# Kernel tuning notes

Hardware: AMD Instinct MI355X
Metric: run time of the kernel (lower is better)

The kernel has to match this reference:

```python
import jax, jax.numpy as jnp
import numpy as np

B, C, D, H = 2, 1024, 1024, 16
DH = D // H
EPS = 1e-8


def setup_inputs() -> dict:
    key = jax.random.key(0)
    ks = jax.random.split(key, 12)
    s = 0.02
    return {
        "x": jax.random.normal(ks[0], (B, C, D), dtype=jnp.float32),
        "rms_w": jnp.ones((C, D), dtype=jnp.float32),
        "rms_b": jnp.zeros((C, D), dtype=jnp.float32),
        "Wqkv": jax.random.normal(ks[1], (3 * D, D), dtype=jnp.float32) * s,
        "Wout": jax.random.normal(ks[2], (D, D), dtype=jnp.float32) * s,
        "bout": jnp.zeros((D,), dtype=jnp.float32),
        "Wf": jax.random.normal(ks[3], (D, D), dtype=jnp.float32) * s,
        "bf": jnp.zeros((D,), dtype=jnp.float32),
        "Ww": jax.random.normal(ks[4], (D, D), dtype=jnp.float32) * s,
        "bw": jnp.zeros((D,), dtype=jnp.float32),
        "Wv": jax.random.normal(ks[5], (D, D), dtype=jnp.float32) * s,
        "bv": jnp.zeros((D,), dtype=jnp.float32),
        "beta": jnp.ones((1,), dtype=jnp.float32),
    }


def _rope_cos_sin(C, dh):
    # faithful to source: theta = 10000 ** (-2*(i-1)/dh), i in [0, dh//2)
    i = jnp.arange(dh // 2, dtype=jnp.float32)
    theta = 10000.0 ** (-2.0 * (i - 1.0) / dh)            # [dh//2]
    ang = jnp.arange(C, dtype=jnp.float32)[:, None] * theta  # [C, dh//2]
    return jnp.cos(ang), jnp.sin(ang)


def _rotate(t, cos, sin):
    # equivalent to einsum('bhci,cij->bhcj', t, R) with the source R
    ev, od = t[..., 0::2], t[..., 1::2]          # [B,H,C,dh//2]
    out_ev = ev * cos + od * sin
    out_od = -ev * sin + od * cos
    return jnp.stack([out_ev, out_od], axis=-1).reshape(t.shape)


def _rmsnorm(x, w, b):
    rms = jnp.sqrt(jnp.mean(x * x, axis=-1, keepdims=True) + EPS)
    return w * (x / rms) + b


def _attention(x, Wqkv, Wout, bout):
    qkv = x @ Wqkv.T                               # [B,C,3D]
    q, k, v = jnp.split(qkv, 3, axis=-1)
    def heads(t):
        return t.reshape(B, C, H, DH).transpose(0, 2, 1, 3)  # [B,H,C,dh]
    q, k, v = heads(q), heads(k), heads(v)
    cos, sin = _rope_cos_sin(C, DH)
    qr = _rotate(q, cos, sin)
    kr = _rotate(k, cos, sin)
    scale = 1.0 / jnp.sqrt(jnp.float32(DH))
    num = jnp.exp(jnp.einsum('bhid,bhjd->bhij', qr, kr) * scale)
    den = jnp.sum(jnp.exp(jnp.einsum('bhid,bhjd->bhij', q, k) * scale),
                  axis=-1, keepdims=True)
    attn = num / den
    mask = jnp.tril(jnp.ones((C, C), dtype=bool))
    attn = jnp.where(mask[None, None], attn, 0.0)
    y = attn @ v                                   # [B,H,C,dh]
    y = y.transpose(0, 2, 1, 3).reshape(B, C, D)
    return y @ Wout.T + bout


def _ffn(x, Wf, bf, Ww, bw, Wv, bv, beta):
    h = x @ Wf.T + bf
    wx = h @ Ww.T + bw
    swish = wx * jax.nn.sigmoid(beta * wx)
    return swish * (h @ Wv.T + bv)


def reference(x, rms_w, rms_b, Wqkv, Wout, bout, Wf, bf, Ww, bw, Wv, bv, beta):
    # dropout p is identity in eval mode
    x = _rmsnorm(x, rms_w, rms_b)
    x = x + _attention(x, Wqkv, Wout, bout)
    x = _rmsnorm(x, rms_w, rms_b)   # same shared RMSNorm module applied twice
    x = x + _ffn(x, Wf, bf, Ww, bw, Wv, bv, beta)
    return x
```

## Files before the change

### kernel.cpp

```cpp
#include <hip/hip_runtime.h>
#include <math.h>

#define B_ 2
#define C_ 1024
#define D_ 1024
#define H_ 16
#define DH_ 64
#define EPSF 1e-8f
#define BK 64

typedef __bf16 bf16;
typedef __attribute__((ext_vector_type(4))) __bf16 bf16x4;
typedef __attribute__((ext_vector_type(8))) __bf16 bf16x8;
typedef __attribute__((ext_vector_type(4))) float f32x4;

__device__ inline f32x4 mfma16(bf16x8 a, bf16x8 b, f32x4 c) {
  return __builtin_amdgcn_mfma_f32_16x16x32_bf16(a, b, c, 0, 0, 0);
}

__device__ inline void async16(const bf16* g, bf16* l) {
  __builtin_amdgcn_global_load_lds((const __attribute__((address_space(1))) void*)g,
                                   (__attribute__((address_space(3))) void*)l, 16, 0, 0);
}

__device__ inline float rope_theta(float i) {
  return exp2f(-13.287712379549449f * (2.0f * (i - 1.0f) * (1.0f / 64.0f)));
}

__global__ __launch_bounds__(256) void cvt_rms_kernel(const float* __restrict__ wqkv,
                                                      const float* __restrict__ wout,
                                                      const float* __restrict__ wf,
                                                      const float* __restrict__ www,
                                                      const float* __restrict__ wv,
                                                      bf16* __restrict__ wdst,
                                                      const float* __restrict__ x,
                                                      const float* __restrict__ rw,
                                                      const float* __restrict__ rb,
                                                      bf16* __restrict__ xout) {
  __shared__ float red[4];
  int t = threadIdx.x;
  if (blockIdx.x < 7 * 1024) {
    int seg = blockIdx.x >> 10;
    int local = (blockIdx.x & 1023) * 1024 + t * 4;
    const float* src = seg < 3 ? wqkv + (size_t)seg * (D_ * D_)
                     : seg == 3 ? wout : seg == 4 ? wf : seg == 5 ? www : wv;
    float4 v = *(const float4*)(src + local);
    bf16x4 o;
    o[0] = (bf16)v.x; o[1] = (bf16)v.y; o[2] = (bf16)v.z; o[3] = (bf16)v.w;
    *(bf16x4*)(wdst + (size_t)seg * (D_ * D_) + local) = o;
    return;
  }
  int row = blockIdx.x - 7 * 1024;
  int c = row & (C_ - 1);
  float4 xv = *(const float4*)(x + (size_t)row * D_ + t * 4);
  float ss = xv.x * xv.x + xv.y * xv.y + xv.z * xv.z + xv.w * xv.w;
#pragma unroll
  for (int m = 1; m < 64; m <<= 1) ss += __shfl_xor(ss, m, 64);
  if ((t & 63) == 0) red[t >> 6] = ss;
  __syncthreads();
  float tot = red[0] + red[1] + red[2] + red[3];
  float inv = rsqrtf(tot * (1.0f / D_) + EPSF);
  float4 wv4 = *(const float4*)(rw + (size_t)c * D_ + t * 4);
  float4 bv4 = *(const float4*)(rb + (size_t)c * D_ + t * 4);
  bf16x4 ov;
  ov[0] = (bf16)(wv4.x * (xv.x * inv) + bv4.x);
  ov[1] = (bf16)(wv4.y * (xv.y * inv) + bv4.y);
  ov[2] = (bf16)(wv4.z * (xv.z * inv) + bv4.z);
  ov[3] = (bf16)(wv4.w * (xv.w * inv) + bv4.w);
  *(bf16x4*)(xout + (size_t)row * D_ + t * 4) = ov;
}

__global__ __launch_bounds__(256) void rmsnorm_bf16_kernel(const bf16* __restrict__ x,
                                                           const float* __restrict__ w,
                                                           const float* __restrict__ b,
                                                           bf16* __restrict__ out) {
  int row = blockIdx.x;
  int c = row & (C_ - 1);
  int t = threadIdx.x;
  bf16x4 xv = *(const bf16x4*)(x + (size_t)row * D_ + t * 4);
  float f0 = (float)xv[0], f1 = (float)xv[1], f2 = (float)xv[2], f3 = (float)xv[3];
  float ss = f0 * f0 + f1 * f1 + f2 * f2 + f3 * f3;
#pragma unroll
  for (int m = 1; m < 64; m <<= 1) ss += __shfl_xor(ss, m, 64);
  __shared__ float red[4];
  if ((t & 63) == 0) red[t >> 6] = ss;
  __syncthreads();
  float tot = red[0] + red[1] + red[2] + red[3];
  float inv = rsqrtf(tot * (1.0f / D_) + EPSF);
  float4 wv = *(const float4*)(w + (size_t)c * D_ + t * 4);
  float4 bv = *(const float4*)(b + (size_t)c * D_ + t * 4);
  bf16x4 ov;
  ov[0] = (bf16)(wv.x * (f0 * inv) + bv.x);
  ov[1] = (bf16)(wv.y * (f1 * inv) + bv.y);
  ov[2] = (bf16)(wv.z * (f2 * inv) + bv.z);
  ov[3] = (bf16)(wv.w * (f3 * inv) + bv.w);
  *(bf16x4*)(out + (size_t)row * D_ + t * 4) = ov;
}

template <int BMt, int BNt>
__global__ __launch_bounds__(256) void gemm_lds(const bf16* __restrict__ A,
                                                const bf16* __restrict__ W,
                                                const float* __restrict__ bias,
                                                const bf16* __restrict__ R,
                                                bf16* __restrict__ Cout,
                                                int M, int N, int K) {
  constexpr int MT = BMt / 32;
  constexpr int NT = BNt / 32;
  __shared__ bf16 sa[BMt * BK];
  __shared__ bf16 sb[BNt * BK];
  int t = threadIdx.x, l = t & 63, w = t >> 6;
  int m0 = blockIdx.y * BMt;
  int n0 = blockIdx.x * BNt;
  int wm = (w >> 1) * (BMt / 2), wn = (w & 1) * (BNt / 2);
  int lm = l & 15, lq = l >> 4;
  int sw = lm & 7;
  f32x4 acc[MT][NT] = {};

  for (int k0 = 0; k0 < K; k0 += BK) {
    __syncthreads();
#pragma unroll
    for (int p = 0; p < BMt / 32; ++p) {
      int lin = p * 256 + t;
      int r = lin >> 3, cc = (lin & 7) ^ (r & 7);
      async16(A + (size_t)(m0 + r) * K + k0 + cc * 8, sa + lin * 8);
    }
#pragma unroll
    for (int p = 0; p < BNt / 32; ++p) {
      int lin = p * 256 + t;
      int r = lin >> 3, cc = (lin & 7) ^ (r & 7);
      async16(W + (size_t)(n0 + r) * K + k0 + cc * 8, sb + lin * 8);
    }
    __syncthreads();
    bf16x8 af[MT][2], bfr[NT][2];
#pragma unroll
    for (int mt = 0; mt < MT; ++mt) {
      const bf16* base = sa + (wm + mt * 16 + lm) * BK;
      af[mt][0] = *(const bf16x8*)(base + ((lq ^ sw) << 3));
      af[mt][1] = *(const bf16x8*)(base + (((4 | lq) ^ sw) << 3));
    }
#pragma unroll
    for (int nt = 0; nt < NT; ++nt) {
      const bf16* base = sb + (wn + nt * 16 + lm) * BK;
      bfr[nt][0] = *(const bf16x8*)(base + ((lq ^ sw) << 3));
      bfr[nt][1] = *(const bf16x8*)(base + (((4 | lq) ^ sw) << 3));
    }
#pragma unroll
    for (int mt = 0; mt < MT; ++mt)
#pragma unroll
      for (int nt = 0; nt < NT; ++nt) {
        acc[mt][nt] = mfma16(af[mt][0], bfr[nt][0], acc[mt][nt]);
        acc[mt][nt] = mfma16(af[mt][1], bfr[nt][1], acc[mt][nt]);
      }
  }
#pragma unroll
  for (int mt = 0; mt < MT; ++mt)
#pragma unroll
    for (int nt = 0; nt < NT; ++nt) {
      int col = n0 + wn + nt * 16 + lm;
      float bb = bias ? bias[col] : 0.0f;
#pragma unroll
      for (int r = 0; r < 4; ++r) {
        int row = m0 + wm + mt * 16 + lq * 4 + r;
        float v = acc[mt][nt][r] + bb;
        if (R) v += (float)R[(size_t)row * N + col];
        Cout[(size_t)row * N + col] = (bf16)v;
      }
    }
}

__global__ __launch_bounds__(256) void gemm_qkv_kernel(const bf16* __restrict__ A,
                                                       const bf16* __restrict__ W,
                                                       bf16* __restrict__ qkv,
                                                       bf16* __restrict__ vt) {
  constexpr int BMt = 128, BNt = 64, MT = 4, NT = 2;
  const int N = 3 * D_, K = D_;
  __shared__ bf16 sa[BMt * BK];
  __shared__ bf16 sb[BNt * BK];
  __shared__ bf16 tv[64 * 136];
  int t = threadIdx.x, l = t & 63, w = t >> 6;
  int m0 = blockIdx.y * BMt;
  int n0 = blockIdx.x * BNt;
  int wm = (w >> 1) * 64, wn = (w & 1) * 32;
  int lm = l & 15, lq = l >> 4;
  int sw = lm & 7;
  f32x4 acc[MT][NT] = {};

  for (int k0 = 0; k0 < K; k0 += BK) {
    __syncthreads();
#pragma unroll
    for (int p = 0; p < 4; ++p) {
      int lin = p * 256 + t;
      int r = lin >> 3, cc = (lin & 7) ^ (r & 7);
      async16(A + (size_t)(m0 + r) * K + k0 + cc * 8, sa + lin * 8);
    }
#pragma unroll
    for (int p = 0; p < 2; ++p) {
      int lin = p * 256 + t;
      int r = lin >> 3, cc = (lin & 7) ^ (r & 7);
      async16(W + (size_t)(n0 + r) * K + k0 + cc * 8, sb + lin * 8);
    }
    __syncthreads();
    bf16x8 af[MT][2], bfr[NT][2];
#pragma unroll
    for (int mt = 0; mt < MT; ++mt) {
      const bf16* base = sa + (wm + mt * 16 + lm) * BK;
      af[mt][0] = *(const bf16x8*)(base + ((lq ^ sw) << 3));
      af[mt][1] = *(const bf16x8*)(base + (((4 | lq) ^ sw) << 3));
    }
#pragma unroll
    for (int nt = 0; nt < NT; ++nt) {
      const bf16* base = sb + (wn + nt * 16 + lm) * BK;
      bfr[nt][0] = *(const bf16x8*)(base + ((lq ^ sw) << 3));
      bfr[nt][1] = *(const bf16x8*)(base + (((4 | lq) ^ sw) << 3));
    }
#pragma unroll
    for (int mt = 0; mt < MT; ++mt)
#pragma unroll
      for (int nt = 0; nt < NT; ++nt) {
        acc[mt][nt] = mfma16(af[mt][0], bfr[nt][0], acc[mt][nt]);
        acc[mt][nt] = mfma16(af[mt][1], bfr[nt][1], acc[mt][nt]);
      }
  }
  if (n0 < 2 * D_) {
#pragma unroll
    for (int mt = 0; mt < MT; ++mt)
#pragma unroll
      for (int nt = 0; nt < NT; ++nt) {
        int col = n0 + wn + nt * 16 + lm;
#pragma unroll
        for (int r = 0; r < 4; ++r) {
          int row = m0 + wm + mt * 16 + lq * 4 + r;
          qkv[(size_t)row * N + col] = (bf16)acc[mt][nt][r];
        }
      }
  } else {
#pragma unroll
    for (int mt = 0; mt < MT; ++mt)
#pragma unroll
      for (int nt = 0; nt < NT; ++nt) {
        int dh = wn + nt * 16 + lm;
#pragma unroll
        for (int r = 0; r < 4; ++r)
          tv[dh * 136 + wm + mt * 16 + lq * 4 + r] = (bf16)acc[mt][nt][r];
      }
    __syncthreads();
    int h = (n0 - 2 * D_) >> 6;
    int bb = m0 >> 10;
    int mloc = m0 & 1023;
    size_t vbase = (size_t)((bb * H_ + h) * DH_) * C_;
#pragma unroll
    for (int p = 0; p < 4; ++p) {
      int lin = p * 256 + t;
      int dh = lin >> 4;
      int mm = (lin & 15) * 8;
      *(int4*)(vt + vbase + (size_t)dh * C_ + mloc + mm) = *(int4*)(tv + dh * 136 + mm);
    }
  }
}

__global__ __launch_bounds__(256) void gemm_ffn_kernel(const bf16* __restrict__ A,
                                                       const bf16* __restrict__ Ww,
                                                       const bf16* __restrict__ Wv,
                                                       const float* __restrict__ bw,
                                                       const float* __restrict__ bv,
                                                       const bf16* __restrict__ x3,
                                                       const float* __restrict__ beta_p,
                                                       float* __restrict__ out) {
  __shared__ bf16 sa[64 * BK];
  __shared__ bf16 sb1[64 * BK];
  __shared__ bf16 sb2[64 * BK];
  int t = threadIdx.x, l = t & 63, w = t >> 6;
  int m0 = blockIdx.y * 64, n0 = blockIdx.x * 64;
  int wm = (w >> 1) * 32, wn = (w & 1) * 32;
  int lm = l & 15, lq = l >> 4;
  int sw = lm & 7;
  float beta = beta_p[0];
  f32x4 acc1[2][2] = {}, acc2[2][2] = {};

  for (int k0 = 0; k0 < D_; k0 += BK) {
    __syncthreads();
#pragma unroll
    for (int p = 0; p < 2; ++p) {
      int lin = p * 256 + t;
      int r = lin >> 3, cc = (lin & 7) ^ (r & 7);
      async16(A + (size_t)(m0 + r) * D_ + k0 + cc * 8, sa + lin * 8);
      async16(Ww + (size_t)(n0 + r) * D_ + k0 + cc * 8, sb1 + lin * 8);
      async16(Wv + (size_t)(n0 + r) * D_ + k0 + cc * 8, sb2 + lin * 8);
    }
    __syncthreads();
    bf16x8 af[2][2], b1f[2][2], b2f[2][2];
#pragma unroll
    for (int mt = 0; mt < 2; ++mt) {
      const bf16* base = sa + (wm + mt * 16 + lm) * BK;
      af[mt][0] = *(const bf16x8*)(base + ((lq ^ sw) << 3));
      af[mt][1] = *(const bf16x8*)(base + (((4 | lq) ^ sw) << 3));
    }
#pragma unroll
    for (int nt = 0; nt < 2; ++nt) {
      const bf16* base1 = sb1 + (wn + nt * 16 + lm) * BK;
      const bf16* base2 = sb2 + (wn + nt * 16 + lm) * BK;
      b1f[nt][0] = *(const bf16x8*)(base1 + ((lq ^ sw) << 3));
      b1f[nt][1] = *(const bf16x8*)(base1 + (((4 | lq) ^ sw) << 3));
      b2f[nt][0] = *(const bf16x8*)(base2 + ((lq ^ sw) << 3));
      b2f[nt][1] = *(const bf16x8*)(base2 + (((4 | lq) ^ sw) << 3));
    }
#pragma unroll
    for (int mt = 0; mt < 2; ++mt)
#pragma unroll
      for (int nt = 0; nt < 2; ++nt) {
        acc1[mt][nt] = mfma16(af[mt][0], b1f[nt][0], acc1[mt][nt]);
        acc1[mt][nt] = mfma16(af[mt][1], b1f[nt][1], acc1[mt][nt]);
        acc2[mt][nt] = mfma16(af[mt][0], b2f[nt][0], acc2[mt][nt]);
        acc2[mt][nt] = mfma16(af[mt][1], b2f[nt][1], acc2[mt][nt]);
      }
  }
#pragma unroll
  for (int mt = 0; mt < 2; ++mt)
#pragma unroll
    for (int nt = 0; nt < 2; ++nt) {
      int col = n0 + wn + nt * 16 + lm;
      float bbw = bw[col], bbv = bv[col];
#pragma unroll
      for (int r = 0; r < 4; ++r) {
        int row = m0 + wm + mt * 16 + lq * 4 + r;
        float z = acc1[mt][nt][r] + bbw;
        float g = acc2[mt][nt][r] + bbv;
        float sw_ = z / (1.0f + __expf(-beta * z));
        out[(size_t)row * D_ + col] = (float)x3[(size_t)row * D_ + col] + sw_ * g;
      }
    }
}

__global__ __launch_bounds__(256) void attn_kernel(const bf16* __restrict__ qkv,
                                                   const bf16* __restrict__ vt,
                                                   bf16* __restrict__ y) {
  __shared__ bf16 sk[64 * 72];
  __shared__ bf16 skr[64 * 72];
  __shared__ bf16 sv[64 * 72];
  __shared__ bf16 pl[4][16 * 72];
  int t = threadIdx.x, l = t & 63, w = t >> 6;
  int blk = blockIdx.x;
  int idx = blk & 255;
  int it = (blk < 256) ? (idx >> 5) : (15 - (idx >> 5));
  int r5 = idx & 31;
  int b = r5 >> 4;
  int h = r5 & 15;
  int i_base = it * 64 + w * 16;
  int lm = l & 15, lq = l >> 4;
  const float scale = 0.125f;

  size_t hq = (size_t)h * DH_;
  size_t qrow = (size_t)(b * C_ + i_base + lm) * (3 * D_) + hq;
  bf16x8 qp[2], qrf[2];
  float cq = (float)(i_base + lm);
#pragma unroll
  for (int kk = 0; kk < 2; ++kk) {
    qp[kk] = *(const bf16x8*)(qkv + qrow + kk * 32 + lq * 8);
#pragma unroll
    for (int j = 0; j < 4; ++j) {
      float ip = (float)(kk * 16 + lq * 4 + j);
      float ang = cq * rope_theta(ip);
      float sv_, cv_;
      __sincosf(ang, &sv_, &cv_);
      float qe = (float)qp[kk][2 * j], qo = (float)qp[kk][2 * j + 1];
      qrf[kk][2 * j] = (bf16)(qe * cv_ + qo * sv_);
      qrf[kk][2 * j + 1] = (bf16)(qo * cv_ - qe * sv_);
    }
  }

  float den[4] = {0.f, 0.f, 0.f, 0.f};
  f32x4 yacc[4] = {};
  int i_max = i_base + 15;
  size_t kbase = (size_t)(b * C_) * (3 * D_) + D_ + hq;
  size_t vtbase = (size_t)((b * H_ + h) * DH_) * C_;
  int sr = t >> 3;
  int sc = (t & 7) * 8;
  float th0 = rope_theta((float)((sc >> 1) + 0));
  float th1 = rope_theta((float)((sc >> 1) + 1));
  float th2 = rope_theta((float)((sc >> 1) + 2));
  float th3 = rope_theta((float)((sc >> 1) + 3));

  float cA0, sA0, cA1, sA1, cA2, sA2, cA3, sA3;
  float cB0, sB0, cB1, sB1, cB2, sB2, cB3, sB3;
  float C0, S0, C1, S1, C2, S2, C3, S3;
#define INITP(P)                  \
  {                               \
    float a;                      \
    a = (float)(sr)*th##P;        \
    __sincosf(a, &sA##P, &cA##P); \
    a = (float)(32 + sr) * th##P; \
    __sincosf(a, &sB##P, &cB##P); \
    a = 64.0f * th##P;            \
    __sincosf(a, &S##P, &C##P);   \
  }
  INITP(0) INITP(1) INITP(2) INITP(3)
#undef INITP

  int4 pk0, pk1, pv0, pv1;
#define FETCH_TILE(J0)                                                          \
  pk0 = *(const int4*)(qkv + kbase + (size_t)((J0) + sr) * (3 * D_) + sc);      \
  pk1 = *(const int4*)(qkv + kbase + (size_t)((J0) + 32 + sr) * (3 * D_) + sc); \
  pv0 = *(const int4*)(vt + vtbase + (size_t)sr * C_ + (J0) + sc);              \
  pv1 = *(const int4*)(vt + vtbase + (size_t)(32 + sr) * C_ + (J0) + sc);

  FETCH_TILE(0)

  for (int j0 = 0; j0 < C_; j0 += 64) {
    __syncthreads();
    *(int4*)(sk + sr * 72 + sc) = pk0;
    *(int4*)(sk + (32 + sr) * 72 + sc) = pk1;
    *(int4*)(sv + sr * 72 + sc) = pv0;
    *(int4*)(sv + (32 + sr) * 72 + sc) = pv1;
    {
      bf16x8 k0 = *(bf16x8*)&pk0, k1 = *(bf16x8*)&pk1;
      bf16x8 r0, r1;
#define ROT2(KV, RV, CC, SS, J)                           \
  {                                                       \
    float e = (float)KV[2 * J], o = (float)KV[2 * J + 1]; \
    RV[2 * J] = (bf16)(e * CC + o * SS);                  \
    RV[2 * J + 1] = (bf16)(o * CC - e * SS);              \
  }
      ROT2(k0, r0, cA0, sA0, 0) ROT2(k0, r0, cA1, sA1, 1)
      ROT2(k0, r0, cA2, sA2, 2) ROT2(k0, r0, cA3, sA3, 3)
      ROT2(k1, r1, cB0, sB0, 0) ROT2(k1, r1, cB1, sB1, 1)
      ROT2(k1, r1, cB2, sB2, 2) ROT2(k1, r1, cB3, sB3, 3)
#undef ROT2
#define STEP(CX, SX, P)               \
  {                                   \
    float nc = CX * C##P - SX * S##P; \
    SX = SX * C##P + CX * S##P;       \
    CX = nc;                          \
  }
      STEP(cA0, sA0, 0) STEP(cA1, sA1, 1) STEP(cA2, sA2, 2) STEP(cA3, sA3, 3)
      STEP(cB0, sB0, 0) STEP(cB1, sB1, 1) STEP(cB2, sB2, 2) STEP(cB3, sB3, 3)
#undef STEP
      *(int4*)(skr + sr * 72 + sc) = *(int4*)&r0;
      *(int4*)(skr + (32 + sr) * 72 + sc) = *(int4*)&r1;
    }
    __syncthreads();
    if (j0 + 64 < C_) {
      FETCH_TILE(j0 + 64)
    }
#pragma unroll
    for (int js = 0; js < 64; js += 16) {
      bf16x8 kf0 = *(const bf16x8*)(sk + (js + lm) * 72 + lq * 8);
      bf16x8 kf1 = *(const bf16x8*)(sk + (js + lm) * 72 + 32 + lq * 8);
      f32x4 s = {0.f, 0.f, 0.f, 0.f};
      s = mfma16(qp[0], kf0, s);
      s = mfma16(qp[1], kf1, s);
#pragma unroll
      for (int r = 0; r < 4; ++r) den[r] += __expf(s[r] * scale);
    }
    if (j0 <= i_max) {
#pragma unroll
      for (int js = 0; js < 64; js += 16) {
        bf16x8 kf0 = *(const bf16x8*)(skr + (js + lm) * 72 + lq * 8);
        bf16x8 kf1 = *(const bf16x8*)(skr + (js + lm) * 72 + 32 + lq * 8);
        f32x4 s = {0.f, 0.f, 0.f, 0.f};
        s = mfma16(qrf[0], kf0, s);
        s = mfma16(qrf[1], kf1, s);
#pragma unroll
        for (int r = 0; r < 4; ++r) {
          int jg = j0 + js + lm;
          int ig = i_base + lq * 4 + r;
          float p = (jg <= ig) ? __expf(s[r] * scale) : 0.0f;
          pl[w][(lq * 4 + r) * 72 + js + lm] = (bf16)p;
        }
      }
      __builtin_amdgcn_wave_barrier();
      bf16x8 pf0 = *(const bf16x8*)(pl[w] + lm * 72 + lq * 8);
      bf16x8 pf1 = *(const bf16x8*)(pl[w] + lm * 72 + 32 + lq * 8);
#pragma unroll
      for (int tt = 0; tt < 4; ++tt) {
        bf16x8 vf0 = *(const bf16x8*)(sv + (tt * 16 + lm) * 72 + lq * 8);
        bf16x8 vf1 = *(const bf16x8*)(sv + (tt * 16 + lm) * 72 + 32 + lq * 8);
        yacc[tt] = mfma16(pf0, vf0, mfma16(pf1, vf1, yacc[tt]));
      }
      __builtin_amdgcn_wave_barrier();
    }
  }
#undef FETCH_TILE
  float inv[4];
#pragma unroll
  for (int r = 0; r < 4; ++r) {
    float d = den[r];
    d += __shfl_xor(d, 1, 64);
    d += __shfl_xor(d, 2, 64);
    d += __shfl_xor(d, 4, 64);
    d += __shfl_xor(d, 8, 64);
    inv[r] = 1.0f / d;
  }
#pragma unroll
  for (int tt = 0; tt < 4; ++tt)
#pragma unroll
    for (int r = 0; r < 4; ++r) {
      int ig = i_base + lq * 4 + r;
      y[(size_t)(b * C_ + ig) * D_ + hq + tt * 16 + lm] = (bf16)(yacc[tt][r] * inv[r]);
    }
}

extern "C" void kernel_launch(void* const* d_in, const int* in_sizes, int n_in,
                              void* d_out, int out_size, void* d_ws, size_t ws_size,
                              hipStream_t stream) {
  const float* x = (const float*)d_in[0];
  const float* rms_w = (const float*)d_in[1];
  const float* rms_b = (const float*)d_in[2];
  const float* Wqkv = (const float*)d_in[3];
  const float* Wout = (const float*)d_in[4];
  const float* bout = (const float*)d_in[5];
  const float* Wf = (const float*)d_in[6];
  const float* bfp = (const float*)d_in[7];
  const float* Ww = (const float*)d_in[8];
  const float* bw = (const float*)d_in[9];
  const float* Wv = (const float*)d_in[10];
  const float* bv = (const float*)d_in[11];
  const float* beta = (const float*)d_in[12];
  float* out = (float*)d_out;

  bf16* ws = (bf16*)d_ws;
  const size_t DD = (size_t)D_ * D_;
  const size_t MC = (size_t)B_ * C_;
  bf16* wb = ws;
  bf16* x1 = ws + 7 * DD;
  bf16* qkv = ws + 9 * DD;
  bf16* vt = ws + 15 * DD;
  bf16* x2 = ws + 17 * DD;
  bf16* x3 = ws + 19 * DD;
  bf16* hbuf = ws + 21 * DD;
  bf16* y = (bf16*)d_out;

  cvt_rms_kernel<<<7 * 1024 + MC, 256, 0, stream>>>(Wqkv, Wout, Wf, Ww, Wv, wb, x, rms_w,
                                                    rms_b, x1);
  gemm_qkv_kernel<<<dim3(3 * D_ / 64, MC / 128), 256, 0, stream>>>(x1, wb, qkv, vt);
  attn_kernel<<<B_ * H_ * 16, 256, 0, stream>>>(qkv, vt, y);
  gemm_lds<64, 64><<<dim3(D_ / 64, MC / 64), 256, 0, stream>>>(
      y, wb + 3 * DD, bout, x1, x2, MC, D_, D_);
  rmsnorm_bf16_kernel<<<MC, 256, 0, stream>>>(x2, rms_w, rms_b, x3);
  gemm_lds<64, 64><<<dim3(D_ / 64, MC / 64), 256, 0, stream>>>(
      x3, wb + 4 * DD, bfp, nullptr, hbuf, MC, D_, D_);
  gemm_ffn_kernel<<<dim3(D_ / 64, MC / 64), 256, 0, stream>>>(
      hbuf, wb + 5 * DD, wb + 6 * DD, bw, bv, x3, beta, out);
}
```

Measured before the change: 204.8 us.

## Double-buffer LDS tiles in the GEMM kernels to overlap loads with MFMA

Converts the generic, QKV and FFN GEMM kernels from single-buffered to double-buffered LDS staging. The next K-tile's async global-to-LDS loads are issued before the MFMA work on the current tile, with one barrier per iteration instead of two. The QKV kernel reuses the pooled LDS for its V-transpose staging buffer. The aim is to hide global load latency behind compute, at the cost of more shared memory per block and possibly lower occupancy.

```diff
diff --git a/kernel.cpp b/kernel.cpp
--- a/kernel.cpp
+++ b/kernel.cpp
@@ -106,43 +106,50 @@
                                                 int M, int N, int K) {
   constexpr int MT = BMt / 32;
   constexpr int NT = BNt / 32;
-  __shared__ bf16 sa[BMt * BK];
-  __shared__ bf16 sb[BNt * BK];
+  __shared__ bf16 sa[2][BMt * BK];
+  __shared__ bf16 sb[2][BNt * BK];
   int t = threadIdx.x, l = t & 63, w = t >> 6;
   int m0 = blockIdx.y * BMt;
   int n0 = blockIdx.x * BNt;
   int wm = (w >> 1) * (BMt / 2), wn = (w & 1) * (BNt / 2);
   int lm = l & 15, lq = l >> 4;
-  int sw = lm & 7;
+  int swz = lm & 7;
   f32x4 acc[MT][NT] = {};
 
-  for (int k0 = 0; k0 < K; k0 += BK) {
-    __syncthreads();
+  auto stage = [&](int buf, int k0) {
 #pragma unroll
     for (int p = 0; p < BMt / 32; ++p) {
       int lin = p * 256 + t;
       int r = lin >> 3, cc = (lin & 7) ^ (r & 7);
-      async16(A + (size_t)(m0 + r) * K + k0 + cc * 8, sa + lin * 8);
+      async16(A + (size_t)(m0 + r) * K + k0 + cc * 8, &sa[buf][lin * 8]);
     }
 #pragma unroll
     for (int p = 0; p < BNt / 32; ++p) {
       int lin = p * 256 + t;
       int r = lin >> 3, cc = (lin & 7) ^ (r & 7);
-      async16(W + (size_t)(n0 + r) * K + k0 + cc * 8, sb + lin * 8);
-    }
-    __syncthreads();
+      async16(W + (size_t)(n0 + r) * K + k0 + cc * 8, &sb[buf][lin * 8]);
+    }
+  };
+
+  stage(0, 0);
+  __syncthreads();
+  int cur = 0;
+  for (int k0 = 0; k0 < K; k0 += BK) {
+    if (k0 + BK < K) stage(cur ^ 1, k0 + BK);
+    const bf16* sac = &sa[cur][0];
+    const bf16* sbc = &sb[cur][0];
     bf16x8 af[MT][2], bfr[NT][2];
 #pragma unroll
     for (int mt = 0; mt < MT; ++mt) {
-      const bf16* base = sa + (wm + mt * 16 + lm) * BK;
-      af[mt][0] = *(const bf16x8*)(base + ((lq ^ sw) << 3));
-      af[mt][1] = *(const bf16x8*)(base + (((4 | lq) ^ sw) << 3));
+      const bf16* base = sac + (wm + mt * 16 + lm) * BK;
+      af[mt][0] = *(const bf16x8*)(base + ((lq ^ swz) << 3));
+      af[mt][1] = *(const bf16x8*)(base + (((4 | lq) ^ swz) << 3));
     }
 #pragma unroll
     for (int nt = 0; nt < NT; ++nt) {
-      const bf16* base = sb + (wn + nt * 16 + lm) * BK;
-      bfr[nt][0] = *(const bf16x8*)(base + ((lq ^ sw) << 3));
-      bfr[nt][1] = *(const bf16x8*)(base + (((4 | lq) ^ sw) << 3));
+      const bf16* base = sbc + (wn + nt * 16 + lm) * BK;
+      bfr[nt][0] = *(const bf16x8*)(base + ((lq ^ swz) << 3));
+      bfr[nt][1] = *(const bf16x8*)(base + (((4 | lq) ^ swz) << 3));
     }
 #pragma unroll
     for (int mt = 0; mt < MT; ++mt)
@@ -151,6 +158,8 @@
         acc[mt][nt] = mfma16(af[mt][0], bfr[nt][0], acc[mt][nt]);
         acc[mt][nt] = mfma16(af[mt][1], bfr[nt][1], acc[mt][nt]);
       }
+    __syncthreads();
+    cur ^= 1;
   }
 #pragma unroll
   for (int mt = 0; mt < MT; ++mt)
@@ -174,44 +183,51 @@
                                                        bf16* __restrict__ vt) {
   constexpr int BMt = 128, BNt = 64, MT = 4, NT = 2;
   const int N = 3 * D_, K = D_;
-  __shared__ bf16 sa[BMt * BK];
-  __shared__ bf16 sb[BNt * BK];
-  __shared__ bf16 tv[64 * 136];
+  __shared__ bf16 pool[2 * BMt * BK + 2 * BNt * BK];
   int t = threadIdx.x, l = t & 63, w = t >> 6;
   int m0 = blockIdx.y * BMt;
   int n0 = blockIdx.x * BNt;
   int wm = (w >> 1) * 64, wn = (w & 1) * 32;
   int lm = l & 15, lq = l >> 4;
-  int sw = lm & 7;
+  int swz = lm & 7;
   f32x4 acc[MT][NT] = {};
 
-  for (int k0 = 0; k0 < K; k0 += BK) {
-    __syncthreads();
+  auto stage = [&](int buf, int k0) {
+    bf16* dA = pool + buf * (BMt * BK);
+    bf16* dB = pool + 2 * (BMt * BK) + buf * (BNt * BK);
 #pragma unroll
     for (int p = 0; p < 4; ++p) {
       int lin = p * 256 + t;
       int r = lin >> 3, cc = (lin & 7) ^ (r & 7);
-      async16(A + (size_t)(m0 + r) * K + k0 + cc * 8, sa + lin * 8);
+      async16(A + (size_t)(m0 + r) * K + k0 + cc * 8, dA + lin * 8);
     }
 #pragma unroll
     for (int p = 0; p < 2; ++p) {
       int lin = p * 256 + t;
       int r = lin >> 3, cc = (lin & 7) ^ (r & 7);
-      async16(W + (size_t)(n0 + r) * K + k0 + cc * 8, sb + lin * 8);
-    }
-    __syncthreads();
+      async16(W + (size_t)(n0 + r) * K + k0 + cc * 8, dB + lin * 8);
+    }
+  };
+
+  stage(0, 0);
+  __syncthreads();
+  int cur = 0;
+  for (int k0 = 0; k0 < K; k0 += BK) {
+    if (k0 + BK < K) stage(cur ^ 1, k0 + BK);
+    const bf16* sac = pool + cur * (BMt * BK);
+    const bf16* sbc = pool + 2 * (BMt * BK) + cur * (BNt * BK);
     bf16x8 af[MT][2], bfr[NT][2];
 #pragma unroll
     for (int mt = 0; mt < MT; ++mt) {
-      const bf16* base = sa + (wm + mt * 16 + lm) * BK;
-      af[mt][0] = *(const bf16x8*)(base + ((lq ^ sw) << 3));
-      af[mt][1] = *(const bf16x8*)(base + (((4 | lq) ^ sw) << 3));
+      const bf16* base = sac + (wm + mt * 16 + lm) * BK;
+      af[mt][0] = *(const bf16x8*)(base + ((lq ^ swz) << 3));
+      af[mt][1] = *(const bf16x8*)(base + (((4 | lq) ^ swz) << 3));
     }
 #pragma unroll
     for (int nt = 0; nt < NT; ++nt) {
-      const bf16* base = sb + (wn + nt * 16 + lm) * BK;
-      bfr[nt][0] = *(const bf16x8*)(base + ((lq ^ sw) << 3));
-      bfr[nt][1] = *(const bf16x8*)(base + (((4 | lq) ^ sw) << 3));
+      const bf16* base = sbc + (wn + nt * 16 + lm) * BK;
+      bfr[nt][0] = *(const bf16x8*)(base + ((lq ^ swz) << 3));
+      bfr[nt][1] = *(const bf16x8*)(base + (((4 | lq) ^ swz) << 3));
     }
 #pragma unroll
     for (int mt = 0; mt < MT; ++mt)
@@ -220,6 +236,8 @@
         acc[mt][nt] = mfma16(af[mt][0], bfr[nt][0], acc[mt][nt]);
         acc[mt][nt] = mfma16(af[mt][1], bfr[nt][1], acc[mt][nt]);
       }
+    __syncthreads();
+    cur ^= 1;
   }
   if (n0 < 2 * D_) {
 #pragma unroll
@@ -234,6 +252,7 @@
         }
       }
   } else {
+    bf16* tv = pool;
 #pragma unroll
     for (int mt = 0; mt < MT; ++mt)
 #pragma unroll
@@ -266,43 +285,51 @@
                                                        const bf16* __restrict__ x3,
                                                        const float* __restrict__ beta_p,
                                                        float* __restrict__ out) {
-  __shared__ bf16 sa[64 * BK];
-  __shared__ bf16 sb1[64 * BK];
-  __shared__ bf16 sb2[64 * BK];
+  __shared__ bf16 sa[2][64 * BK];
+  __shared__ bf16 sb1[2][64 * BK];
+  __shared__ bf16 sb2[2][64 * BK];
   int t = threadIdx.x, l = t & 63, w = t >> 6;
   int m0 = blockIdx.y * 64, n0 = blockIdx.x * 64;
   int wm = (w >> 1) * 32, wn = (w & 1) * 32;
   int lm = l & 15, lq = l >> 4;
-  int sw = lm & 7;
+  int swz = lm & 7;
   float beta = beta_p[0];
   f32x4 acc1[2][2] = {}, acc2[2][2] = {};
 
-  for (int k0 = 0; k0 < D_; k0 += BK) {
-    __syncthreads();
+  auto stage = [&](int buf, int k0) {
 #pragma unroll
     for (int p = 0; p < 2; ++p) {
       int lin = p * 256 + t;
       int r = lin >> 3, cc = (lin & 7) ^ (r & 7);
-      async16(A + (size_t)(m0 + r) * D_ + k0 + cc * 8, sa + lin * 8);
-      async16(Ww + (size_t)(n0 + r) * D_ + k0 + cc * 8, sb1 + lin * 8);
-      async16(Wv + (size_t)(n0 + r) * D_ + k0 + cc * 8, sb2 + lin * 8);
-    }
-    __syncthreads();
+      async16(A + (size_t)(m0 + r) * D_ + k0 + cc * 8, &sa[buf][lin * 8]);
+      async16(Ww + (size_t)(n0 + r) * D_ + k0 + cc * 8, &sb1[buf][lin * 8]);
+      async16(Wv + (size_t)(n0 + r) * D_ + k0 + cc * 8, &sb2[buf][lin * 8]);
+    }
+  };
+
+  stage(0, 0);
+  __syncthreads();
+  int cur = 0;
+  for (int k0 = 0; k0 < D_; k0 += BK) {
+    if (k0 + BK < D_) stage(cur ^ 1, k0 + BK);
+    const bf16* sac = &sa[cur][0];
+    const bf16* sb1c = &sb1[cur][0];
+    const bf16* sb2c = &sb2[cur][0];
     bf16x8 af[2][2], b1f[2][2], b2f[2][2];
 #pragma unroll
     for (int mt = 0; mt < 2; ++mt) {
-      const bf16* base = sa + (wm + mt * 16 + lm) * BK;
-      af[mt][0] = *(const bf16x8*)(base + ((lq ^ sw) << 3));
-      af[mt][1] = *(const bf16x8*)(base + (((4 | lq) ^ sw) << 3));
+      const bf16* base = sac + (wm + mt * 16 + lm) * BK;
+      af[mt][0] = *(const bf16x8*)(base + ((lq ^ swz) << 3));
+      af[mt][1] = *(const bf16x8*)(base + (((4 | lq) ^ swz) << 3));
     }
 #pragma unroll
     for (int nt = 0; nt < 2; ++nt) {
-      const bf16* base1 = sb1 + (wn + nt * 16 + lm) * BK;
-      const bf16* base2 = sb2 + (wn + nt * 16 + lm) * BK;
-      b1f[nt][0] = *(const bf16x8*)(base1 + ((lq ^ sw) << 3));
-      b1f[nt][1] = *(const bf16x8*)(base1 + (((4 | lq) ^ sw) << 3));
-      b2f[nt][0] = *(const bf16x8*)(base2 + ((lq ^ sw) << 3));
-      b2f[nt][1] = *(const bf16x8*)(base2 + (((4 | lq) ^ sw) << 3));
+      const bf16* base1 = sb1c + (wn + nt * 16 + lm) * BK;
+      const bf16* base2 = sb2c + (wn + nt * 16 + lm) * BK;
+      b1f[nt][0] = *(const bf16x8*)(base1 + ((lq ^ swz) << 3));
+      b1f[nt][1] = *(const bf16x8*)(base1 + (((4 | lq) ^ swz) << 3));
+      b2f[nt][0] = *(const bf16x8*)(base2 + ((lq ^ swz) << 3));
+      b2f[nt][1] = *(const bf16x8*)(base2 + (((4 | lq) ^ swz) << 3));
     }
 #pragma unroll
     for (int mt = 0; mt < 2; ++mt)
@@ -313,6 +340,8 @@
         acc2[mt][nt] = mfma16(af[mt][0], b2f[nt][0], acc2[mt][nt]);
         acc2[mt][nt] = mfma16(af[mt][1], b2f[nt][1], acc2[mt][nt]);
       }
+    __syncthreads();
+    cur ^= 1;
   }
 #pragma unroll
   for (int mt = 0; mt < 2; ++mt)
```

New measurement: 211.2 us. +3.1%, slower.
